# Kernel optimization log

Hardware: AMD Instinct MI355X
Metric: run time of the kernel (lower is better)

The kernel has to match this reference:

```python
import jax, jax.numpy as jnp
import numpy as np
import math

IN_DIM = 512
PARAM_DIM = 512
OUT_DIM = 2048
GROUPS = 4
COMPRESS = 4
PLANES = OUT_DIM // COMPRESS          # 512
GROUP_PLANES = PLANES // GROUPS       # 128
ATTN_SCALE = PLANES ** (-0.5)         # note: full planes, as in the source
N, L = 16, 1024
M = L  # required by sv.reshape(N, planes, L)


def equal_linear(x, w, b, in_dim):
    # EqualLinear: F.linear(x, w * (1/sqrt(in_dim)) * lr_mul, bias * lr_mul), lr_mul=1
    scale = 1.0 / math.sqrt(in_dim)
    return jnp.einsum('nlc,oc->nlo', x, w * scale) + b


def setup_inputs() -> dict:
    key = jax.random.key(0)
    ks = jax.random.split(key, 8)
    return {
        'attention': jax.random.normal(ks[0], (N, L, IN_DIM), dtype=jnp.float32),
        'op_param': jax.random.normal(ks[1], (N, M, PARAM_DIM), dtype=jnp.float32),
        'q_w': jax.random.normal(ks[2], (PLANES, PARAM_DIM), dtype=jnp.float32),
        'q_b': jnp.zeros((PLANES,), dtype=jnp.float32),
        'k_w': jax.random.normal(ks[3], (PLANES, IN_DIM), dtype=jnp.float32),
        'k_b': jnp.zeros((PLANES,), dtype=jnp.float32),
        'v_w': jax.random.normal(ks[4], (PLANES, IN_DIM), dtype=jnp.float32),
        'v_b': jnp.zeros((PLANES,), dtype=jnp.float32),
        'proj_w': jax.random.normal(ks[5], (OUT_DIM, PLANES), dtype=jnp.float32),
        'proj_b': jnp.zeros((OUT_DIM,), dtype=jnp.float32),
    }


def reference(attention, op_param, q_w, q_b, k_w, k_b, v_w, v_b, proj_w, proj_b):
    n, l, _ = attention.shape
    m = op_param.shape[1]
    # q/k/v: (N, T, planes) -> (N, groups, group_planes, T)
    q = equal_linear(op_param, q_w, q_b, PARAM_DIM).reshape(n, m, GROUPS, GROUP_PLANES).transpose(0, 2, 3, 1)
    k = equal_linear(attention, k_w, k_b, IN_DIM).reshape(n, l, GROUPS, GROUP_PLANES).transpose(0, 2, 3, 1)
    v = equal_linear(attention, v_w, v_b, IN_DIM).reshape(n, l, GROUPS, GROUP_PLANES).transpose(0, 2, 3, 1)
    # scores: (N, groups, M, L)
    qk = jnp.einsum('ngdm,ngdl->ngml', q, k) * ATTN_SCALE
    sim = jax.nn.softmax(qk, axis=3)
    # sv: (N, groups, group_planes, M)
    sv = jnp.einsum('ngml,ngdl->ngdm', sim, v)
    # (N, planes, L) -> (N, L, planes); valid because M == L
    stacked = sv.reshape(n, PLANES, l).transpose(0, 2, 1)
    out = equal_linear(stacked, proj_w, proj_b, PLANES)
    return out
```

## Files before the change

### kernel.cpp

```cpp
#include <hip/hip_runtime.h>
#include <hip/hip_bf16.h>

#define NB 16
#define TT 1024
#define CC 512
#define PP 512
#define GG 4
#define DD 128
#define OO 2048

#define SCL 0.04419417382415922f

typedef __attribute__((ext_vector_type(8))) short short8;
typedef __attribute__((ext_vector_type(4))) float floatx4;
#define MFMA(a, b, c) __builtin_amdgcn_mfma_f32_16x16x32_bf16((a), (b), (c), 0, 0, 0)

static __device__ __forceinline__ float bf2f(unsigned short u) {
  union { unsigned int i; float f; } v; v.i = ((unsigned int)u) << 16; return v.f;
}
static __device__ __forceinline__ unsigned short f2bf(float f) {
  union { float f; unsigned int i; } v; v.f = f;
  unsigned int r = (v.i + 0x7fffu + ((v.i >> 16) & 1u)) >> 16;
  return (unsigned short)r;
}
static __device__ __forceinline__ ushort4 pack4(float4 v) {
  ushort4 o; o.x = f2bf(v.x); o.y = f2bf(v.y); o.z = f2bf(v.z); o.w = f2bf(v.w); return o;
}

template <int VLAY>
__global__ __launch_bounds__(256) void k_proj(
    const float* __restrict__ x, const float* __restrict__ w,
    const float* __restrict__ b, unsigned short* __restrict__ y) {
  __shared__ unsigned short Aw[128][32];
  __shared__ unsigned short Xw[128][32];
  const int n  = blockIdx.z;
  const int p0 = blockIdx.y * 128;
  const int t0 = blockIdx.x * 128;
  const int tid  = threadIdx.x;
  const int wave = tid >> 6, lane = tid & 63;
  const int l15  = lane & 15, quad = lane >> 4;
  const int wm = (wave >> 1) * 64, wn = (wave & 1) * 64;
  const int srow = tid >> 3, scol = (tid & 7) * 4;
  const float* xn = x + (size_t)n * TT * CC;
  floatx4 acc[4][4] = {};

  for (int k0 = 0; k0 < CC; k0 += 32) {
    float4 aw[4], ax[4];
#pragma unroll
    for (int q = 0; q < 4; ++q) {
      aw[q] = *reinterpret_cast<const float4*>(w  + (size_t)(p0 + srow + q * 32) * CC + k0 + scol);
      ax[q] = *reinterpret_cast<const float4*>(xn + (size_t)(t0 + srow + q * 32) * CC + k0 + scol);
    }
    __syncthreads();
#pragma unroll
    for (int q = 0; q < 4; ++q) {
      *reinterpret_cast<ushort4*>(&Aw[srow + q * 32][scol]) = pack4(aw[q]);
      *reinterpret_cast<ushort4*>(&Xw[srow + q * 32][scol]) = pack4(ax[q]);
    }
    __syncthreads();
    short8 af[4], bx[4];
#pragma unroll
    for (int mt = 0; mt < 4; ++mt)
      af[mt] = *reinterpret_cast<const short8*>(&Aw[wm + mt * 16 + l15][quad * 8]);
#pragma unroll
    for (int nt = 0; nt < 4; ++nt)
      bx[nt] = *reinterpret_cast<const short8*>(&Xw[wn + nt * 16 + l15][quad * 8]);
#pragma unroll
    for (int mt = 0; mt < 4; ++mt)
#pragma unroll
      for (int nt = 0; nt < 4; ++nt)
        acc[mt][nt] = MFMA(af[mt], bx[nt], acc[mt][nt]);
  }

#pragma unroll
  for (int mt = 0; mt < 4; ++mt) {
    const int pb = p0 + wm + mt * 16 + quad * 4;
    const float4 bias = *reinterpret_cast<const float4*>(b + pb);
    const float bb[4] = {bias.x, bias.y, bias.z, bias.w};
#pragma unroll
    for (int nt = 0; nt < 4; ++nt) {
      const int tc = t0 + wn + nt * 16 + l15;
      if (VLAY == 0) {
        ushort4 o;
        o.x = f2bf(acc[mt][nt][0] * SCL + bb[0]);
        o.y = f2bf(acc[mt][nt][1] * SCL + bb[1]);
        o.z = f2bf(acc[mt][nt][2] * SCL + bb[2]);
        o.w = f2bf(acc[mt][nt][3] * SCL + bb[3]);
        *reinterpret_cast<ushort4*>(y + ((size_t)n * TT + tc) * PP + pb) = o;
      } else {
#pragma unroll
        for (int r = 0; r < 4; ++r)
          y[((size_t)n * PP + pb + r) * TT + tc] = f2bf(acc[mt][nt][r] * SCL + bb[r]);
      }
    }
  }
}

__global__ __launch_bounds__(256) void k_attn(
    const unsigned short* __restrict__ Q,
    const unsigned short* __restrict__ K,
    const unsigned short* __restrict__ V,
    unsigned short* __restrict__ SV) {
  __shared__ unsigned short Sc[32][1032];
  __shared__ float rowinv[32];
  const int lin = blockIdx.x;
  const int wu  = (lin >> 3) | ((lin & 7) << 8);
  const int m0 = (wu & 31) * 32;
  const int g  = (wu >> 5) & 3;
  const int n  = wu >> 7;
  const int tid  = threadIdx.x;
  const int wave = tid >> 6, lane = tid & 63;
  const int l15  = lane & 15, quad = lane >> 4;

  const unsigned short* Qn = Q + (size_t)n * TT * PP;
  const unsigned short* Kn = K + (size_t)n * TT * PP;
  const unsigned short* Vn = V + ((size_t)n * PP + g * DD) * TT;

  short8 aq[2][4];
#pragma unroll
  for (int mt = 0; mt < 2; ++mt)
#pragma unroll
    for (int ds = 0; ds < 4; ++ds)
      aq[mt][ds] = *reinterpret_cast<const short8*>(
          Qn + (size_t)(m0 + mt * 16 + l15) * PP + g * DD + ds * 32 + quad * 8);

#pragma unroll
  for (int pass = 0; pass < 4; ++pass) {
    short8 bk[4][4];
#pragma unroll
    for (int ds = 0; ds < 4; ++ds)
#pragma unroll
      for (int j = 0; j < 4; ++j)
        bk[ds][j] = *reinterpret_cast<const short8*>(
            Kn + (size_t)(pass * 256 + (wave * 4 + j) * 16 + l15) * PP +
            g * DD + ds * 32 + quad * 8);
    floatx4 acc[2][4] = {};
#pragma unroll
    for (int ds = 0; ds < 4; ++ds)
#pragma unroll
      for (int j = 0; j < 4; ++j) {
        acc[0][j] = MFMA(aq[0][ds], bk[ds][j], acc[0][j]);
        acc[1][j] = MFMA(aq[1][ds], bk[ds][j], acc[1][j]);
      }
#pragma unroll
    for (int mt = 0; mt < 2; ++mt)
#pragma unroll
      for (int j = 0; j < 4; ++j) {
        const int lc = pass * 256 + (wave * 4 + j) * 16 + l15;
#pragma unroll
        for (int r = 0; r < 4; ++r)
          Sc[mt * 16 + quad * 4 + r][lc] = f2bf(acc[mt][j][r] * SCL);
      }
  }
  __syncthreads();

  {
    const int mi = tid >> 3;
    const int j  = tid & 7;
    unsigned short* row = &Sc[mi][0];
    float mx = -1e30f;
#pragma unroll
    for (int i = 0; i < 16; ++i) {
      short8 u = *reinterpret_cast<const short8*>(&row[(i * 8 + j) * 8]);
      float a0 = fmaxf(bf2f((unsigned short)u[0]), bf2f((unsigned short)u[1]));
      float a1 = fmaxf(bf2f((unsigned short)u[2]), bf2f((unsigned short)u[3]));
      float a2 = fmaxf(bf2f((unsigned short)u[4]), bf2f((unsigned short)u[5]));
      float a3 = fmaxf(bf2f((unsigned short)u[6]), bf2f((unsigned short)u[7]));
      mx = fmaxf(mx, fmaxf(fmaxf(a0, a1), fmaxf(a2, a3)));
    }
#pragma unroll
    for (int off = 4; off; off >>= 1) mx = fmaxf(mx, __shfl_xor(mx, off, 8));
    float sum = 0.f;
#pragma unroll
    for (int i = 0; i < 16; ++i) {
      short8 u = *reinterpret_cast<short8*>(&row[(i * 8 + j) * 8]);
      short8 o;
      float s0 = 0.f, s1 = 0.f;
#pragma unroll
      for (int e = 0; e < 8; e += 2) {
        float e0 = __expf(bf2f((unsigned short)u[e])     - mx);
        float e1 = __expf(bf2f((unsigned short)u[e + 1]) - mx);
        s0 += e0; s1 += e1;
        o[e]     = (short)f2bf(e0);
        o[e + 1] = (short)f2bf(e1);
      }
      sum += s0 + s1;
      *reinterpret_cast<short8*>(&row[(i * 8 + j) * 8]) = o;
    }
#pragma unroll
    for (int off = 4; off; off >>= 1) sum += __shfl_xor(sum, off, 8);
    if (j == 0) rowinv[mi] = 1.f / sum;
  }
  __syncthreads();

  floatx4 av[2][2] = {};
#pragma unroll 4
  for (int ls = 0; ls < 32; ++ls) {
    short8 va[2], bp[2];
#pragma unroll
    for (int a = 0; a < 2; ++a)
      va[a] = *reinterpret_cast<const short8*>(
          Vn + (size_t)(wave * 32 + a * 16 + l15) * TT + ls * 32 + quad * 8);
#pragma unroll
    for (int mt = 0; mt < 2; ++mt)
      bp[mt] = *reinterpret_cast<const short8*>(&Sc[mt * 16 + l15][ls * 32 + quad * 8]);
#pragma unroll
    for (int a = 0; a < 2; ++a)
#pragma unroll
      for (int mt = 0; mt < 2; ++mt)
        av[a][mt] = MFMA(va[a], bp[mt], av[a][mt]);
  }
#pragma unroll
  for (int a = 0; a < 2; ++a) {
    const int pb = g * DD + wave * 32 + a * 16 + quad * 4;
#pragma unroll
    for (int mt = 0; mt < 2; ++mt) {
      const float inv = rowinv[mt * 16 + l15];
      ushort4 o;
      o.x = f2bf(av[a][mt][0] * inv);
      o.y = f2bf(av[a][mt][1] * inv);
      o.z = f2bf(av[a][mt][2] * inv);
      o.w = f2bf(av[a][mt][3] * inv);
      *reinterpret_cast<ushort4*>(
          SV + ((size_t)n * TT + m0 + mt * 16 + l15) * PP + pb) = o;
    }
  }
}

__global__ __launch_bounds__(256) void k_out(
    const unsigned short* __restrict__ SVp, const float* __restrict__ w,
    const float* __restrict__ b, float* __restrict__ out) {
  __shared__ unsigned short Wt[128][32];
  __shared__ unsigned short St[128][32];
  const int lin = blockIdx.x;
  const int wu  = (lin >> 3) | ((lin & 7) << 8);
  const int t0 = (wu & 7) * 128;
  const int o0 = ((wu >> 3) & 15) * 128;
  const int n  = wu >> 7;
  const int tid  = threadIdx.x;
  const int wave = tid >> 6, lane = tid & 63;
  const int l15  = lane & 15, quad = lane >> 4;
  const int wm = (wave >> 1) * 64, wn = (wave & 1) * 64;
  const int srow = tid >> 3, scol = (tid & 7) * 4;
  const unsigned short* SVn = SVp + (size_t)n * TT * PP;
  floatx4 acc[4][4] = {};

  for (int k0 = 0; k0 < PP; k0 += 32) {
    float4 awf[4];
    ushort4 us[4];
#pragma unroll
    for (int q = 0; q < 4; ++q) {
      awf[q] = *reinterpret_cast<const float4*>(w + (size_t)(o0 + srow + q * 32) * PP + k0 + scol);
      us[q]  = *reinterpret_cast<const ushort4*>(SVn + (size_t)(t0 + srow + q * 32) * PP + k0 + scol);
    }
    __syncthreads();
#pragma unroll
    for (int q = 0; q < 4; ++q) {
      *reinterpret_cast<ushort4*>(&Wt[srow + q * 32][scol]) = pack4(awf[q]);
      *reinterpret_cast<ushort4*>(&St[srow + q * 32][scol]) = us[q];
    }
    __syncthreads();
    short8 af[4], bs[4];
#pragma unroll
    for (int mt = 0; mt < 4; ++mt)
      af[mt] = *reinterpret_cast<const short8*>(&Wt[wm + mt * 16 + l15][quad * 8]);
#pragma unroll
    for (int nt = 0; nt < 4; ++nt)
      bs[nt] = *reinterpret_cast<const short8*>(&St[wn + nt * 16 + l15][quad * 8]);
#pragma unroll
    for (int mt = 0; mt < 4; ++mt)
#pragma unroll
      for (int nt = 0; nt < 4; ++nt)
        acc[mt][nt] = MFMA(af[mt], bs[nt], acc[mt][nt]);
  }

#pragma unroll
  for (int mt = 0; mt < 4; ++mt) {
    const int ob = o0 + wm + mt * 16 + quad * 4;
    const float4 bias = *reinterpret_cast<const float4*>(b + ob);
    const float bb[4] = {bias.x, bias.y, bias.z, bias.w};
#pragma unroll
    for (int nt = 0; nt < 4; ++nt) {
      const int tc = t0 + wn + nt * 16 + l15;
      float4 o;
      o.x = acc[mt][nt][0] * SCL + bb[0];
      o.y = acc[mt][nt][1] * SCL + bb[1];
      o.z = acc[mt][nt][2] * SCL + bb[2];
      o.w = acc[mt][nt][3] * SCL + bb[3];
      *reinterpret_cast<float4*>(out + ((size_t)n * TT + tc) * OO + ob) = o;
    }
  }
}

extern "C" void kernel_launch(void* const* d_in, const int* in_sizes, int n_in,
                              void* d_out, int out_size, void* d_ws, size_t ws_size,
                              hipStream_t stream) {
  (void)in_sizes; (void)n_in; (void)out_size; (void)ws_size;
  const float* attention = (const float*)d_in[0];
  const float* op_param  = (const float*)d_in[1];
  const float* q_w = (const float*)d_in[2];
  const float* q_b = (const float*)d_in[3];
  const float* k_w = (const float*)d_in[4];
  const float* k_b = (const float*)d_in[5];
  const float* v_w = (const float*)d_in[6];
  const float* v_b = (const float*)d_in[7];
  const float* proj_w = (const float*)d_in[8];
  const float* proj_b = (const float*)d_in[9];
  float* out = (float*)d_out;

  const size_t NPT = (size_t)NB * PP * TT;
  unsigned short* scratch = (unsigned short*)d_out;
  unsigned short* Qw  = scratch;
  unsigned short* Kw  = scratch + NPT;
  unsigned short* Vw  = scratch + 2 * NPT;
  unsigned short* SVw = (unsigned short*)d_ws;

  dim3 blk(256);
  dim3 gp(TT / 128, PP / 128, NB);
  k_proj<0><<<gp, blk, 0, stream>>>(op_param,  q_w, q_b, Qw);
  k_proj<0><<<gp, blk, 0, stream>>>(attention, k_w, k_b, Kw);
  k_proj<1><<<gp, blk, 0, stream>>>(attention, v_w, v_b, Vw);
  k_attn<<<dim3(2048), blk, 0, stream>>>(Qw, Kw, Vw, SVw);
  k_out<<<dim3(2048), blk, 0, stream>>>(SVw, proj_w, proj_b, out);
}
```

Before: 457.2 us.

## Software-pipeline K and V loads in attention kernel, simplify output grid mapping

The attention kernel now double-buffers K fragments across the four score passes and keeps a four-deep rotating register prefetch of V fragments in the PV loop, so global loads overlap the MFMA work. It also adds a min-blocks-per-CU hint to launch bounds. The output-projection kernel drops the XCD-swizzled 1D block index for a plain 3D grid, and bf16 rounding now uses the library conversion. The extra live registers may push against the occupancy hint or cause spills, and removing the swizzle may change L2 locality.

Result: faster. 447.1 us (-2.2%).

```diff
diff --git a/kernel.cpp b/kernel.cpp
--- a/kernel.cpp
+++ b/kernel.cpp
@@ -19,9 +19,8 @@
   union { unsigned int i; float f; } v; v.i = ((unsigned int)u) << 16; return v.f;
 }
 static __device__ __forceinline__ unsigned short f2bf(float f) {
-  union { float f; unsigned int i; } v; v.f = f;
-  unsigned int r = (v.i + 0x7fffu + ((v.i >> 16) & 1u)) >> 16;
-  return (unsigned short)r;
+  __hip_bfloat16 h = __float2bfloat16(f);
+  return *reinterpret_cast<unsigned short*>(&h);
 }
 static __device__ __forceinline__ ushort4 pack4(float4 v) {
   ushort4 o; o.x = f2bf(v.x); o.y = f2bf(v.y); o.z = f2bf(v.z); o.w = f2bf(v.w); return o;
@@ -96,7 +95,7 @@
   }
 }
 
-__global__ __launch_bounds__(256) void k_attn(
+__global__ __launch_bounds__(256, 2) void k_attn(
     const unsigned short* __restrict__ Q,
     const unsigned short* __restrict__ K,
     const unsigned short* __restrict__ V,
@@ -124,16 +123,16 @@
       aq[mt][ds] = *reinterpret_cast<const short8*>(
           Qn + (size_t)(m0 + mt * 16 + l15) * PP + g * DD + ds * 32 + quad * 8);
 
-#pragma unroll
-  for (int pass = 0; pass < 4; ++pass) {
-    short8 bk[4][4];
+  auto kload = [&](short8 (&dst)[4][4], int base_l) {
 #pragma unroll
     for (int ds = 0; ds < 4; ++ds)
 #pragma unroll
       for (int j = 0; j < 4; ++j)
-        bk[ds][j] = *reinterpret_cast<const short8*>(
-            Kn + (size_t)(pass * 256 + (wave * 4 + j) * 16 + l15) * PP +
+        dst[ds][j] = *reinterpret_cast<const short8*>(
+            Kn + (size_t)(base_l + (wave * 4 + j) * 16 + l15) * PP +
             g * DD + ds * 32 + quad * 8);
+  };
+  auto kcomp = [&](const short8 (&bk)[4][4], int base_l) {
     floatx4 acc[2][4] = {};
 #pragma unroll
     for (int ds = 0; ds < 4; ++ds)
@@ -146,12 +145,22 @@
     for (int mt = 0; mt < 2; ++mt)
 #pragma unroll
       for (int j = 0; j < 4; ++j) {
-        const int lc = pass * 256 + (wave * 4 + j) * 16 + l15;
+        const int lc = base_l + (wave * 4 + j) * 16 + l15;
 #pragma unroll
         for (int r = 0; r < 4; ++r)
           Sc[mt * 16 + quad * 4 + r][lc] = f2bf(acc[mt][j][r] * SCL);
       }
-  }
+  };
+
+  short8 bkA[4][4], bkB[4][4];
+  kload(bkA, 0);
+  kload(bkB, 256);
+  kcomp(bkA, 0);
+  kload(bkA, 512);
+  kcomp(bkB, 256);
+  kload(bkB, 768);
+  kcomp(bkA, 512);
+  kcomp(bkB, 768);
   __syncthreads();
 
   {
@@ -194,13 +203,14 @@
   __syncthreads();
 
   floatx4 av[2][2] = {};
-#pragma unroll 4
-  for (int ls = 0; ls < 32; ++ls) {
-    short8 va[2], bp[2];
+  auto vload = [&](short8 (&dst)[2], int ls) {
 #pragma unroll
     for (int a = 0; a < 2; ++a)
-      va[a] = *reinterpret_cast<const short8*>(
+      dst[a] = *reinterpret_cast<const short8*>(
           Vn + (size_t)(wave * 32 + a * 16 + l15) * TT + ls * 32 + quad * 8);
+  };
+  auto vstep = [&](const short8 (&va)[2], int ls) {
+    short8 bp[2];
 #pragma unroll
     for (int mt = 0; mt < 2; ++mt)
       bp[mt] = *reinterpret_cast<const short8*>(&Sc[mt * 16 + l15][ls * 32 + quad * 8]);
@@ -209,7 +219,18 @@
 #pragma unroll
       for (int mt = 0; mt < 2; ++mt)
         av[a][mt] = MFMA(va[a], bp[mt], av[a][mt]);
-  }
+  };
+
+  short8 va0[2], va1[2], va2[2], va3[2];
+  vload(va0, 0); vload(va1, 1); vload(va2, 2); vload(va3, 3);
+#pragma unroll
+  for (int ls = 0; ls < 32; ls += 4) {
+    vstep(va0, ls);     if (ls + 4 < 32) vload(va0, ls + 4);
+    vstep(va1, ls + 1); if (ls + 5 < 32) vload(va1, ls + 5);
+    vstep(va2, ls + 2); if (ls + 6 < 32) vload(va2, ls + 6);
+    vstep(va3, ls + 3); if (ls + 7 < 32) vload(va3, ls + 7);
+  }
+
 #pragma unroll
   for (int a = 0; a < 2; ++a) {
     const int pb = g * DD + wave * 32 + a * 16 + quad * 4;
@@ -232,11 +253,9 @@
     const float* __restrict__ b, float* __restrict__ out) {
   __shared__ unsigned short Wt[128][32];
   __shared__ unsigned short St[128][32];
-  const int lin = blockIdx.x;
-  const int wu  = (lin >> 3) | ((lin & 7) << 8);
-  const int t0 = (wu & 7) * 128;
-  const int o0 = ((wu >> 3) & 15) * 128;
-  const int n  = wu >> 7;
+  const int n  = blockIdx.z;
+  const int o0 = blockIdx.y * 128;
+  const int t0 = blockIdx.x * 128;
   const int tid  = threadIdx.x;
   const int wave = tid >> 6, lane = tid & 63;
   const int l15  = lane & 15, quad = lane >> 4;
@@ -321,5 +340,5 @@
   k_proj<0><<<gp, blk, 0, stream>>>(attention, k_w, k_b, Kw);
   k_proj<1><<<gp, blk, 0, stream>>>(attention, v_w, v_b, Vw);
   k_attn<<<dim3(2048), blk, 0, stream>>>(Qw, Kw, Vw, SVw);
-  k_out<<<dim3(2048), blk, 0, stream>>>(SVw, proj_w, proj_b, out);
-}
+  k_out<<<dim3(TT / 128, OO / 128, NB), blk, 0, stream>>>(SVw, proj_w, proj_b, out);
+}
```
